# Kernel optimization log

Measured on AMD Instinct MI355X. Metric: run time of the kernel, lower is better.

The kernel has to match this reference:

```python
import jax, jax.numpy as jnp
import numpy as np

B, N, DIM = 4, 16384, 256
H, D, G = 8, 64, 32  # heads, dim_head, slice_num; inner = H*D = 512


def setup_inputs() -> dict:
    key = jax.random.key(0)
    ks = jax.random.split(key, 12)
    inner = H * D
    s = lambda fan_in: 1.0 / np.sqrt(fan_in)
    inp = {
        "x": jax.random.normal(ks[0], (B, N, DIM), jnp.float32),
        # weights stored (in, out) so forward is x @ W + b
        "Wfx": jax.random.uniform(ks[1], (DIM, inner), jnp.float32, -s(DIM), s(DIM)),
        "bfx": jnp.zeros((inner,), jnp.float32),
        "Wx": jax.random.uniform(ks[2], (DIM, inner), jnp.float32, -s(DIM), s(DIM)),
        "bx": jnp.zeros((inner,), jnp.float32),
        "Wslice": jnp.linalg.qr(jax.random.normal(ks[3], (D, G), jnp.float32))[0],  # orthogonal init
        "bslice": jnp.zeros((G,), jnp.float32),
        "temperature": jnp.full((1, H, 1, 1), 0.5, jnp.float32),
        "Wq": jax.random.uniform(ks[4], (D, D), jnp.float32, -s(D), s(D)),
        "Wk": jax.random.uniform(ks[5], (D, D), jnp.float32, -s(D), s(D)),
        "Wv": jax.random.uniform(ks[6], (D, D), jnp.float32, -s(D), s(D)),
        "Wout": jax.random.uniform(ks[7], (inner, DIM), jnp.float32, -s(inner), s(inner)),
        "bout": jnp.zeros((DIM,), jnp.float32),
    }
    return inp


def reference(x, Wfx, bfx, Wx, bx, Wslice, bslice, temperature, Wq, Wk, Wv, Wout, bout):
    b, n, _ = x.shape
    # projections -> [B, H, N, D]
    fx_mid = (x @ Wfx + bfx).reshape(b, n, H, D).transpose(0, 2, 1, 3)
    x_mid = (x @ Wx + bx).reshape(b, n, H, D).transpose(0, 2, 1, 3)
    # soft slice assignment: [B, H, N, G]
    slice_logits = (x_mid @ Wslice + bslice) / temperature
    slice_weights = jax.nn.softmax(slice_logits, axis=-1)
    slice_norm = slice_weights.sum(axis=2)  # [B, H, G]
    # soft pooling to G slice tokens: [B, H, G, D]
    slice_token = jnp.einsum("bhnd,bhng->bhgd", fx_mid, slice_weights)
    slice_token = slice_token / (slice_norm[..., None] + 1e-5)
    # tiny attention over G tokens
    q = slice_token @ Wq
    k = slice_token @ Wk
    v = slice_token @ Wv
    scores = jnp.einsum("bhgd,bhkd->bhgk", q, k) / jnp.sqrt(jnp.asarray(D, q.dtype))
    attn = jax.nn.softmax(scores, axis=-1)
    out_slice = jnp.einsum("bhgk,bhkd->bhgd", attn, v)
    # scatter back to N points: [B, H, N, D] -> [B, N, H*D]
    out_x = jnp.einsum("bhgd,bhng->bhnd", out_slice, slice_weights)
    out_x = out_x.transpose(0, 2, 1, 3).reshape(b, n, H * D)
    return out_x @ Wout + bout
```

## Files before the change

### kernel.cpp

```cpp
#include <hip/hip_runtime.h>


typedef unsigned short u16;
typedef __attribute__((ext_vector_type(8))) unsigned short ushort8v;
typedef __attribute__((ext_vector_type(4))) unsigned short ushort4v;
typedef __attribute__((ext_vector_type(8))) short short8v;
typedef __attribute__((ext_vector_type(4))) float f32x4;

constexpr int Nc = 16384;
constexpr int BNc = 65536;

__device__ inline float b2f(u16 v) {
    union { unsigned int u; float f; } t; t.u = ((unsigned int)v) << 16; return t.f;
}
__device__ inline u16 f2b(float f) {
    union { float f; unsigned int u; } t; t.f = f;
    unsigned int u = t.u;
    return (u16)((u + 0x7fffu + ((u >> 16) & 1u)) >> 16);
}

__global__ __launch_bounds__(256) void k0_fold(
    const float* __restrict__ Wx, const float* __restrict__ Wslice,
    const float* __restrict__ bx, const float* __restrict__ bslice,
    u16* __restrict__ WxsT, float* __restrict__ bxs)
{
    int blk = blockIdx.x, tid = threadIdx.x;
    int h = tid >> 5, g = tid & 31;
    if (blk < 256) {
        int k = blk;
        float acc = 0.f;
        for (int d = 0; d < 64; d++)
            acc += Wx[k * 512 + h * 64 + d] * Wslice[d * 32 + g];
        WxsT[tid * 256 + k] = f2b(acc);
    } else {
        float acc = 0.f;
        for (int d = 0; d < 64; d++)
            acc += bx[h * 64 + d] * Wslice[d * 32 + g];
        bxs[tid] = acc + bslice[g];
    }
}

__global__ __launch_bounds__(256) void kprep_wfx(const float* __restrict__ Wfx,
                                                 u16* __restrict__ WfxT)
{
    int n = blockIdx.x, k = threadIdx.x;
    WfxT[n * 256 + k] = f2b(Wfx[k * 512 + n]);
}

__global__ __launch_bounds__(256) void kfrag(const u16* __restrict__ Ball,
                                             u16* __restrict__ Bf)
{
    int g = blockIdx.x * 256 + threadIdx.x;
    int pair = g >> 6, lane = g & 63;
    int t = pair >> 3, c = pair & 7;
    int n = t * 16 + (lane & 15);
    int k = c * 32 + (lane >> 4) * 8;
    ushort8v v = *(const ushort8v*)(Ball + (size_t)n * 256 + k);
    *(ushort8v*)(Bf + (size_t)((c * 48 + t) * 64 + lane) * 8) = v;
}

__global__ __launch_bounds__(256, 4) void kproj(
    const float* __restrict__ x, const u16* __restrict__ Bf,
    const float* __restrict__ bfx, const float* __restrict__ bxs,
    const float* __restrict__ temp,
    u16* __restrict__ fxT, u16* __restrict__ swb, u16* __restrict__ swT)
{
    __shared__ u16 Bs[2][12288];
    int tid = threadIdx.x;
    int wave = tid >> 6, lane = tid & 63;
    int lm = lane & 15, quad = lane >> 4;
    int wr = wave & 1, wc = wave >> 1;
    int cg = blockIdx.y;
    int row0 = blockIdx.x * 32;
    int arow = row0 + wr * 16 + lm;

    const float* Aptr = x + (size_t)arow * 256 + quad * 8;
    const u16* BfW = Bf + (size_t)cg * 12288 + (size_t)(wave * 6) * 512 + lane * 8;

    f32x4 acc[12] = {};
    f32x4 a0 = *(const f32x4*)(Aptr);
    f32x4 a1 = *(const f32x4*)(Aptr + 4);

#pragma unroll
    for (int i = 0; i < 6; i++)
        __builtin_amdgcn_global_load_lds((const uint32_t*)(BfW + i * 512),
                                         (uint32_t*)(&Bs[0][(wave * 6 + i) * 512]),
                                         16, 0, 0);
    __syncthreads();

    int cur = 0;
    for (int c = 0; c < 8; c++) {
        if (c < 7) {
            const u16* src = BfW + (size_t)(c + 1) * 24576;
            u16* dst = &Bs[cur ^ 1][(wave * 6) * 512];
#pragma unroll
            for (int i = 0; i < 6; i++)
                __builtin_amdgcn_global_load_lds((const uint32_t*)(src + i * 512),
                                                 (uint32_t*)(dst + i * 512), 16, 0, 0);
        }
        ushort8v au;
#pragma unroll
        for (int j = 0; j < 4; j++) { au[j] = f2b(a0[j]); au[4 + j] = f2b(a1[j]); }
        short8v af = (short8v&)au;
        if (c < 7) {
            a0 = *(const f32x4*)(Aptr + c * 32 + 32);
            a1 = *(const f32x4*)(Aptr + c * 32 + 36);
        }
#pragma unroll
        for (int j = 0; j < 12; j++) {
            short8v bf = *(short8v*)&Bs[cur][(wc * 12 + j) * 512 + lane * 8];
            acc[j] = __builtin_amdgcn_mfma_f32_16x16x32_bf16(af, bf, acc[j], 0, 0, 0);
        }
        __syncthreads();
        cur ^= 1;
    }

    int nbase = row0 + wr * 16 + quad * 4;
    int tbase = cg * 24 + wc * 12;
    int nfx = (cg == 0) ? 12 : (wc == 0 ? 8 : 0);
#pragma unroll
    for (int j = 0; j < 12; j++) {
        if (j < nfx) {
            int cc = (tbase + j) * 16 + lm;
            float bv = bfx[cc];
            ushort4v o;
#pragma unroll
            for (int r = 0; r < 4; r++) o[r] = f2b(acc[j][r] + bv);
            *(ushort4v*)(fxT + (size_t)cc * 65536 + nbase) = o;
        }
    }

    if (cg == 1) {
        int b = row0 >> 14;
        int nlbase = (row0 & 16383) + wr * 16 + quad * 4;
        int nh = wc ? 6 : 2, h0 = wc ? 2 : 0, jb = wc ? 0 : 8;
#pragma unroll
        for (int hh = 0; hh < 6; hh++) {
            if (hh < nh) {
                int h = h0 + hh;
                float it = 1.0f / temp[h];
                float bv0 = bxs[h * 32 + lm];
                float bv1 = bxs[h * 32 + 16 + lm];
                f32x4 A0 = acc[jb + 2 * hh];
                f32x4 A1 = acc[jb + 2 * hh + 1];
                ushort4v p0, p1;
#pragma unroll
                for (int r = 0; r < 4; r++) {
                    float v0 = (A0[r] + bv0) * it;
                    float v1 = (A1[r] + bv1) * it;
                    float m = fmaxf(v0, v1);
                    m = fmaxf(m, __shfl_xor(m, 1));
                    m = fmaxf(m, __shfl_xor(m, 2));
                    m = fmaxf(m, __shfl_xor(m, 4));
                    m = fmaxf(m, __shfl_xor(m, 8));
                    float e0 = __expf(v0 - m), e1 = __expf(v1 - m);
                    float s = e0 + e1;
                    s += __shfl_xor(s, 1);
                    s += __shfl_xor(s, 2);
                    s += __shfl_xor(s, 4);
                    s += __shfl_xor(s, 8);
                    float rs = 1.0f / s;
                    float w0 = e0 * rs, w1 = e1 * rs;
                    int row = row0 + wr * 16 + quad * 4 + r;
                    swb[(size_t)row * 256 + h * 32 + lm] = f2b(w0);
                    swb[(size_t)row * 256 + h * 32 + 16 + lm] = f2b(w1);
                    p0[r] = f2b(w0); p1[r] = f2b(w1);
                }
                size_t gbase = (size_t)((b * 8 + h) * 32);
                *(ushort4v*)(swT + (gbase + lm) * 16384 + nlbase) = p0;
                *(ushort4v*)(swT + (gbase + 16 + lm) * 16384 + nlbase) = p1;
            }
        }
    }
}

__global__ __launch_bounds__(256, 4) void kout(
    const u16* __restrict__ swb, const u16* __restrict__ ZTf,
    const float* __restrict__ bout, float* __restrict__ out)
{
    __shared__ u16 Bs[16 * 512];
    int tid = threadIdx.x;
    int wave = tid >> 6, lane = tid & 63;
    int lm = lane & 15, quad = lane >> 4;
    int row0 = blockIdx.x * 64;

    const u16* Abase = swb + (size_t)(row0 + wave * 16 + lm) * 256 + quad * 8;
    const u16* Zb    = ZTf + (size_t)(row0 >> 14) * 65536;

    f32x4 acc[16] = {};
    short8v af = *(const short8v*)(Abase);
    for (int c = 0; c < 8; c++) {
        const u16* src = Zb + (size_t)c * 8192 + (size_t)(wave * 4) * 512 + lane * 8;
#pragma unroll
        for (int i = 0; i < 4; i++) {
            ushort8v v = *(const ushort8v*)(src + i * 512);
            *(ushort8v*)&Bs[(wave * 4 + i) * 512 + lane * 8] = v;
        }
        short8v a_cur = af;
        if (c < 7) af = *(const short8v*)(Abase + c * 32 + 32);
        __syncthreads();
#pragma unroll
        for (int j = 0; j < 16; j++) {
            short8v bf = *(short8v*)&Bs[j * 512 + lane * 8];
            acc[j] = __builtin_amdgcn_mfma_f32_16x16x32_bf16(a_cur, bf, acc[j], 0, 0, 0);
        }
        __syncthreads();
    }
#pragma unroll
    for (int j = 0; j < 16; j++) {
        int cc = j * 16 + lm;
        float bv = bout[cc];
#pragma unroll
        for (int r = 0; r < 4; r++)
            out[(size_t)(row0 + wave * 16 + quad * 4 + r) * 256 + cc] = acc[j][r] + bv;
    }
}

__global__ __launch_bounds__(256, 4) void k4_token_mfma(
    const u16* __restrict__ swT, const u16* __restrict__ fxT,
    float* __restrict__ token_part, float* __restrict__ norm_part)
{
    __shared__ u16 As[32 * 256];
    __shared__ u16 Bs_[64 * 256];
    int bh = blockIdx.x, ky = blockIdx.y;
    int b = bh >> 3, h = bh & 7;
    int tid = threadIdx.x, wave = tid >> 6, lane = tid & 63;
    int lm = lane & 15, quad = lane >> 4;
    int mt = wave & 1, dp = wave >> 1;
    int lh = lane >> 5, lb = lane & 31;

#pragma unroll
    for (int i = 0; i < 4; i++) {
        int s = wave * 4 + i;
        int r = 2 * s + lh;
        int sw = ((lb * 16) ^ ((r & 7) << 4)) >> 1;
        const u16* src = swT + (size_t)(bh * 32 + r) * 16384 + ky * 256 + sw;
        __builtin_amdgcn_global_load_lds((const uint32_t*)src,
                                         (uint32_t*)(&As[s * 512]), 16, 0, 0);
    }
#pragma unroll
    for (int i = 0; i < 8; i++) {
        int s = wave * 8 + i;
        int r = 2 * s + lh;
        int sw = ((lb * 16) ^ ((r & 7) << 4)) >> 1;
        const u16* src = fxT + (size_t)(h * 64 + r) * 65536 + (size_t)b * 16384
                         + ky * 256 + sw;
        __builtin_amdgcn_global_load_lds((const uint32_t*)src,
                                         (uint32_t*)(&Bs_[s * 512]), 16, 0, 0);
    }
    __syncthreads();

    int rA = mt * 16 + lm;
    int rB0 = dp * 32 + lm, rB1 = rB0 + 16;
    const char* Ab  = (const char*)As  + rA  * 512;
    const char* Bb0 = (const char*)Bs_ + rB0 * 512;
    const char* Bb1 = (const char*)Bs_ + rB1 * 512;
    int swA  = (rA  & 7) << 4;
    int swB0 = (rB0 & 7) << 4;
    int swB1 = (rB1 & 7) << 4;

    f32x4 acc0 = {}, acc1 = {};
    float nacc = 0.f;
#pragma unroll
    for (int kk = 0; kk < 8; kk++) {
        int base = kk * 64 + quad * 16;
        short8v af = *(const short8v*)(Ab  + (base ^ swA));
        short8v b0 = *(const short8v*)(Bb0 + (base ^ swB0));
        short8v b1 = *(const short8v*)(Bb1 + (base ^ swB1));
        acc0 = __builtin_amdgcn_mfma_f32_16x16x32_bf16(af, b0, acc0, 0, 0, 0);
        acc1 = __builtin_amdgcn_mfma_f32_16x16x32_bf16(af, b1, acc1, 0, 0, 0);
        if (dp == 0) {
            ushort8v au = (ushort8v&)af;
#pragma unroll
            for (int j = 0; j < 8; j++) nacc += b2f(au[j]);
        }
    }
    float* tp = token_part + ((size_t)(ky * 32 + bh)) * 2048;
#pragma unroll
    for (int r = 0; r < 4; r++) {
        int g = mt * 16 + quad * 4 + r;
        tp[g * 64 + dp * 32 + lm] = acc0[r];
        tp[g * 64 + dp * 32 + 16 + lm] = acc1[r];
    }
    if (dp == 0) {
        nacc += __shfl_xor(nacc, 16);
        nacc += __shfl_xor(nacc, 32);
        if (lane < 16)
            norm_part[(ky * 32 + bh) * 32 + mt * 16 + lm] = nacc;
    }
}

__global__ __launch_bounds__(256) void k4b_reduce(
    const float* __restrict__ tp, const float* __restrict__ np,
    float* __restrict__ tl)
{
    int t = blockIdx.x * 256 + threadIdx.x;
    int bh = t >> 11, e = t & 2047, g = e >> 6;
    float ts = 0.f, ns = 0.f;
    for (int ch = 0; ch < 64; ch++) {
        ts += tp[((size_t)(ch * 32 + bh)) * 2048 + e];
        ns += np[(ch * 32 + bh) * 32 + g];
    }
    tl[t] = ts / (ns + 1e-5f);
}

__global__ __launch_bounds__(256) void k5_attn(
    const float* __restrict__ tlg,
    const float* __restrict__ Wq, const float* __restrict__ Wk, const float* __restrict__ Wv,
    float* __restrict__ out_slice)
{
    __shared__ float tl[32][64];
    __shared__ float ql[32][64], kl[32][64], vl[32][64];
    __shared__ float sl[32][33];
    int bh = blockIdx.x, tid = threadIdx.x;
    const float* tk = tlg + (size_t)bh * 2048;

#pragma unroll
    for (int j = 0; j < 8; j++) {
        int idx = j * 256 + tid;
        tl[idx >> 6][idx & 63] = tk[idx];
    }
    __syncthreads();
#pragma unroll
    for (int j = 0; j < 8; j++) {
        int idx = j * 256 + tid;
        int g = idx >> 6, d = idx & 63;
        float aq = 0.f, ak = 0.f, av = 0.f;
        for (int e = 0; e < 64; e++) {
            float t = tl[g][e];
            aq += t * Wq[e * 64 + d];
            ak += t * Wk[e * 64 + d];
            av += t * Wv[e * 64 + d];
        }
        ql[g][d] = aq; kl[g][d] = ak; vl[g][d] = av;
    }
    __syncthreads();
#pragma unroll
    for (int j = 0; j < 4; j++) {
        int idx = j * 256 + tid;
        int gq = idx >> 5, gk = idx & 31;
        float s = 0.f;
        for (int d = 0; d < 64; d++) s += ql[gq][d] * kl[gk][d];
        sl[gq][gk] = s * 0.125f;
    }
    __syncthreads();
    if (tid < 32) {
        float m = -1e30f;
        for (int k2 = 0; k2 < 32; k2++) m = fmaxf(m, sl[tid][k2]);
        float s = 0.f;
        for (int k2 = 0; k2 < 32; k2++) { float e = __expf(sl[tid][k2] - m); sl[tid][k2] = e; s += e; }
        float r = 1.0f / s;
        for (int k2 = 0; k2 < 32; k2++) sl[tid][k2] *= r;
    }
    __syncthreads();
#pragma unroll
    for (int j = 0; j < 8; j++) {
        int idx = j * 256 + tid;
        int g = idx >> 6, d = idx & 63;
        float a = 0.f;
        for (int k2 = 0; k2 < 32; k2++) a += sl[g][k2] * vl[k2][d];
        out_slice[(size_t)bh * 2048 + idx] = a;
    }
}

__global__ __launch_bounds__(256) void kZ(
    const float* __restrict__ os, const float* __restrict__ Wout,
    u16* __restrict__ ZTf)
{
    int b = blockIdx.x, cb = blockIdx.y;
    int t = threadIdx.x;
    int c = cb * 16 + (t & 15), kq = t >> 4;
    int tile = c >> 4, lm = c & 15;
    for (int k = kq * 16; k < kq * 16 + 16; k++) {
        int h = k >> 5, g = k & 31;
        const float* osr = os + ((size_t)(b * 8 + h)) * 2048 + g * 64;
        float acc = 0.f;
        for (int d = 0; d < 64; d++)
            acc += osr[d] * Wout[(h * 64 + d) * 256 + c];
        int ch = k >> 5, quad = (k >> 3) & 3, jj = k & 7;
        int lane = quad * 16 + lm;
        ZTf[((size_t)((b * 8 + ch) * 16 + tile)) * 512 + lane * 8 + jj] = f2b(acc);
    }
}

extern "C" void kernel_launch(void* const* d_in, const int* in_sizes, int n_in,
                              void* d_out, int out_size, void* d_ws, size_t ws_size,
                              hipStream_t stream)
{
    const float* x      = (const float*)d_in[0];
    const float* Wfx    = (const float*)d_in[1];
    const float* bfx    = (const float*)d_in[2];
    const float* Wx     = (const float*)d_in[3];
    const float* bx     = (const float*)d_in[4];
    const float* Wslice = (const float*)d_in[5];
    const float* bslice = (const float*)d_in[6];
    const float* temp   = (const float*)d_in[7];
    const float* Wq     = (const float*)d_in[8];
    const float* Wk     = (const float*)d_in[9];
    const float* Wv     = (const float*)d_in[10];
    const float* Wout   = (const float*)d_in[11];
    const float* bout   = (const float*)d_in[12];

    char* ws = (char*)d_ws;
    size_t off = 0;
    auto alloc = [&](size_t bytes) {
        void* p = ws + off;
        off = (off + bytes + 255) & ~(size_t)255;
        return p;
    };
    u16*   fxT   = (u16*)  alloc((size_t)512 * BNc * 2);
    u16*   swb   = (u16*)  alloc((size_t)BNc * 256 * 2);
    u16*   swT   = (u16*)  alloc((size_t)1024 * Nc * 2);
    float* tp    = (float*)alloc((size_t)2048 * 2048 * 4);
    float* np    = (float*)alloc((size_t)2048 * 32 * 4);
    float* tl    = (float*)alloc(65536 * 4);
    float* osl   = (float*)alloc(65536 * 4);
    u16*   ZTf   = (u16*)  alloc(4 * 65536 * 2);
    u16*   Ball  = (u16*)  alloc((size_t)768 * 256 * 2);
    u16*   Bfrg  = (u16*)  alloc((size_t)768 * 256 * 2);
    float* bxs   = (float*)alloc(256 * 4);

    u16* WfxT = Ball;
    u16* WxsT = Ball + (size_t)512 * 256;

    k0_fold<<<257, 256, 0, stream>>>(Wx, Wslice, bx, bslice, WxsT, bxs);
    kprep_wfx<<<512, 256, 0, stream>>>(Wfx, WfxT);
    kfrag<<<96, 256, 0, stream>>>(Ball, Bfrg);

    kproj<<<dim3(2048, 2), 256, 0, stream>>>(x, Bfrg, bfx, bxs, temp, fxT, swb, swT);

    k4_token_mfma<<<dim3(32, 64), 256, 0, stream>>>(swT, fxT, tp, np);
    k4b_reduce<<<256, 256, 0, stream>>>(tp, np, tl);
    k5_attn<<<32, 256, 0, stream>>>(tl, Wq, Wk, Wv, osl);
    kZ<<<dim3(4, 16), 256, 0, stream>>>(osl, Wout, ZTf);

    kout<<<1024, 256, 0, stream>>>(swb, ZTf, bout, (float*)d_out);
}
```

Baseline: 376.0 us.

## Restructure projection GEMM to keep weights in registers and stage x in swizzled LDS

The projection kernel now uses 512-thread blocks over a 3-way column split. Each wave holds its two B column tiles in registers for the whole K loop, and the 32x256 x tile is converted to bf16 once and stored in XOR-swizzled shared memory. This replaces the double-buffered LDS streaming of weights and the per-wave fp32 A loads with their repeated bf16 conversion. Softmax output is now computed by a dedicated block group with one wave per head. In exchange, x is re-read by three block groups instead of two, and register pressure rises from the 16 held B fragments.

```diff
diff --git a/kernel.cpp b/kernel.cpp
--- a/kernel.cpp
+++ b/kernel.cpp
@@ -59,117 +59,110 @@
     *(ushort8v*)(Bf + (size_t)((c * 48 + t) * 64 + lane) * 8) = v;
 }
 
-__global__ __launch_bounds__(256, 4) void kproj(
+__global__ __launch_bounds__(512, 4) void kproj(
     const float* __restrict__ x, const u16* __restrict__ Bf,
     const float* __restrict__ bfx, const float* __restrict__ bxs,
     const float* __restrict__ temp,
     u16* __restrict__ fxT, u16* __restrict__ swb, u16* __restrict__ swT)
 {
-    __shared__ u16 Bs[2][12288];
+    __shared__ u16 As[32 * 256];
     int tid = threadIdx.x;
     int wave = tid >> 6, lane = tid & 63;
     int lm = lane & 15, quad = lane >> 4;
-    int wr = wave & 1, wc = wave >> 1;
-    int cg = blockIdx.y;
+    int tg = blockIdx.y;
     int row0 = blockIdx.x * 32;
-    int arow = row0 + wr * 16 + lm;
-
-    const float* Aptr = x + (size_t)arow * 256 + quad * 8;
-    const u16* BfW = Bf + (size_t)cg * 12288 + (size_t)(wave * 6) * 512 + lane * 8;
-
-    f32x4 acc[12] = {};
-    f32x4 a0 = *(const f32x4*)(Aptr);
-    f32x4 a1 = *(const f32x4*)(Aptr + 4);
-
-#pragma unroll
-    for (int i = 0; i < 6; i++)
-        __builtin_amdgcn_global_load_lds((const uint32_t*)(BfW + i * 512),
-                                         (uint32_t*)(&Bs[0][(wave * 6 + i) * 512]),
-                                         16, 0, 0);
-    __syncthreads();
-
-    int cur = 0;
+    int T0 = tg * 16 + 2 * wave;
+
+    short8v breg0[8], breg1[8];
+#pragma unroll
     for (int c = 0; c < 8; c++) {
-        if (c < 7) {
-            const u16* src = BfW + (size_t)(c + 1) * 24576;
-            u16* dst = &Bs[cur ^ 1][(wave * 6) * 512];
-#pragma unroll
-            for (int i = 0; i < 6; i++)
-                __builtin_amdgcn_global_load_lds((const uint32_t*)(src + i * 512),
-                                                 (uint32_t*)(dst + i * 512), 16, 0, 0);
-        }
-        ushort8v au;
-#pragma unroll
-        for (int j = 0; j < 4; j++) { au[j] = f2b(a0[j]); au[4 + j] = f2b(a1[j]); }
-        short8v af = (short8v&)au;
-        if (c < 7) {
-            a0 = *(const f32x4*)(Aptr + c * 32 + 32);
-            a1 = *(const f32x4*)(Aptr + c * 32 + 36);
-        }
-#pragma unroll
-        for (int j = 0; j < 12; j++) {
-            short8v bf = *(short8v*)&Bs[cur][(wc * 12 + j) * 512 + lane * 8];
-            acc[j] = __builtin_amdgcn_mfma_f32_16x16x32_bf16(af, bf, acc[j], 0, 0, 0);
-        }
-        __syncthreads();
-        cur ^= 1;
-    }
-
-    int nbase = row0 + wr * 16 + quad * 4;
-    int tbase = cg * 24 + wc * 12;
-    int nfx = (cg == 0) ? 12 : (wc == 0 ? 8 : 0);
-#pragma unroll
-    for (int j = 0; j < 12; j++) {
-        if (j < nfx) {
-            int cc = (tbase + j) * 16 + lm;
+        breg0[c] = *(const short8v*)(Bf + (size_t)((c * 48 + T0) * 64 + lane) * 8);
+        breg1[c] = *(const short8v*)(Bf + (size_t)((c * 48 + T0 + 1) * 64 + lane) * 8);
+    }
+
+    {
+        int row = tid >> 4, colg = tid & 15;
+        const f32x4* src = (const f32x4*)(x + (size_t)(row0 + row) * 256 + colg * 16);
+        f32x4 v0 = src[0], v1 = src[1], v2 = src[2], v3 = src[3];
+        ushort8v o0, o1;
+#pragma unroll
+        for (int j = 0; j < 4; j++) {
+            o0[j] = f2b(v0[j]); o0[4 + j] = f2b(v1[j]);
+            o1[j] = f2b(v2[j]); o1[4 + j] = f2b(v3[j]);
+        }
+        int sw = (row & 7) << 4;
+        char* base = (char*)As + row * 512;
+        *(ushort8v*)(base + ((colg * 32) ^ sw)) = o0;
+        *(ushort8v*)(base + ((colg * 32 + 16) ^ sw)) = o1;
+    }
+    __syncthreads();
+
+    f32x4 acc00 = {}, acc01 = {}, acc10 = {}, acc11 = {};
+    int swl = (lm & 7) << 4;
+    const char* Arow0 = (const char*)As + lm * 512;
+    const char* Arow1 = (const char*)As + (16 + lm) * 512;
+#pragma unroll
+    for (int c = 0; c < 8; c++) {
+        int off = (c * 64 + quad * 16) ^ swl;
+        short8v af0 = *(const short8v*)(Arow0 + off);
+        short8v af1 = *(const short8v*)(Arow1 + off);
+        acc00 = __builtin_amdgcn_mfma_f32_16x16x32_bf16(af0, breg0[c], acc00, 0, 0, 0);
+        acc10 = __builtin_amdgcn_mfma_f32_16x16x32_bf16(af1, breg0[c], acc10, 0, 0, 0);
+        acc01 = __builtin_amdgcn_mfma_f32_16x16x32_bf16(af0, breg1[c], acc01, 0, 0, 0);
+        acc11 = __builtin_amdgcn_mfma_f32_16x16x32_bf16(af1, breg1[c], acc11, 0, 0, 0);
+    }
+
+    if (tg < 2) {
+        int nbase = row0 + quad * 4;
+#pragma unroll
+        for (int i = 0; i < 2; i++) {
+            int cc = (T0 + i) * 16 + lm;
             float bv = bfx[cc];
-            ushort4v o;
-#pragma unroll
-            for (int r = 0; r < 4; r++) o[r] = f2b(acc[j][r] + bv);
-            *(ushort4v*)(fxT + (size_t)cc * 65536 + nbase) = o;
-        }
-    }
-
-    if (cg == 1) {
+            const f32x4& a0 = i ? acc01 : acc00;
+            const f32x4& a1 = i ? acc11 : acc10;
+            ushort4v o0, o1;
+#pragma unroll
+            for (int r = 0; r < 4; r++) { o0[r] = f2b(a0[r] + bv); o1[r] = f2b(a1[r] + bv); }
+            *(ushort4v*)(fxT + (size_t)cc * 65536 + nbase) = o0;
+            *(ushort4v*)(fxT + (size_t)cc * 65536 + nbase + 16) = o1;
+        }
+    } else {
+        int h = wave;
         int b = row0 >> 14;
-        int nlbase = (row0 & 16383) + wr * 16 + quad * 4;
-        int nh = wc ? 6 : 2, h0 = wc ? 2 : 0, jb = wc ? 0 : 8;
-#pragma unroll
-        for (int hh = 0; hh < 6; hh++) {
-            if (hh < nh) {
-                int h = h0 + hh;
-                float it = 1.0f / temp[h];
-                float bv0 = bxs[h * 32 + lm];
-                float bv1 = bxs[h * 32 + 16 + lm];
-                f32x4 A0 = acc[jb + 2 * hh];
-                f32x4 A1 = acc[jb + 2 * hh + 1];
-                ushort4v p0, p1;
-#pragma unroll
-                for (int r = 0; r < 4; r++) {
-                    float v0 = (A0[r] + bv0) * it;
-                    float v1 = (A1[r] + bv1) * it;
-                    float m = fmaxf(v0, v1);
-                    m = fmaxf(m, __shfl_xor(m, 1));
-                    m = fmaxf(m, __shfl_xor(m, 2));
-                    m = fmaxf(m, __shfl_xor(m, 4));
-                    m = fmaxf(m, __shfl_xor(m, 8));
-                    float e0 = __expf(v0 - m), e1 = __expf(v1 - m);
-                    float s = e0 + e1;
-                    s += __shfl_xor(s, 1);
-                    s += __shfl_xor(s, 2);
-                    s += __shfl_xor(s, 4);
-                    s += __shfl_xor(s, 8);
-                    float rs = 1.0f / s;
-                    float w0 = e0 * rs, w1 = e1 * rs;
-                    int row = row0 + wr * 16 + quad * 4 + r;
-                    swb[(size_t)row * 256 + h * 32 + lm] = f2b(w0);
-                    swb[(size_t)row * 256 + h * 32 + 16 + lm] = f2b(w1);
-                    p0[r] = f2b(w0); p1[r] = f2b(w1);
-                }
-                size_t gbase = (size_t)((b * 8 + h) * 32);
-                *(ushort4v*)(swT + (gbase + lm) * 16384 + nlbase) = p0;
-                *(ushort4v*)(swT + (gbase + 16 + lm) * 16384 + nlbase) = p1;
+        float it = 1.0f / temp[h];
+        float bv0 = bxs[h * 32 + lm];
+        float bv1 = bxs[h * 32 + 16 + lm];
+        size_t gbase = (size_t)((b * 8 + h) * 32);
+#pragma unroll
+        for (int rf = 0; rf < 2; rf++) {
+            const f32x4& A0 = rf ? acc10 : acc00;
+            const f32x4& A1 = rf ? acc11 : acc01;
+            int nlbase = (row0 & 16383) + rf * 16 + quad * 4;
+            ushort4v p0, p1;
+#pragma unroll
+            for (int r = 0; r < 4; r++) {
+                float v0 = (A0[r] + bv0) * it;
+                float v1 = (A1[r] + bv1) * it;
+                float m = fmaxf(v0, v1);
+                m = fmaxf(m, __shfl_xor(m, 1));
+                m = fmaxf(m, __shfl_xor(m, 2));
+                m = fmaxf(m, __shfl_xor(m, 4));
+                m = fmaxf(m, __shfl_xor(m, 8));
+                float e0 = __expf(v0 - m), e1 = __expf(v1 - m);
+                float s = e0 + e1;
+                s += __shfl_xor(s, 1);
+                s += __shfl_xor(s, 2);
+                s += __shfl_xor(s, 4);
+                s += __shfl_xor(s, 8);
+                float rs = 1.0f / s;
+                float w0 = e0 * rs, w1 = e1 * rs;
+                int row = row0 + rf * 16 + quad * 4 + r;
+                swb[(size_t)row * 256 + h * 32 + lm] = f2b(w0);
+                swb[(size_t)row * 256 + h * 32 + 16 + lm] = f2b(w1);
+                p0[r] = f2b(w0); p1[r] = f2b(w1);
             }
+            *(ushort4v*)(swT + (gbase + lm) * 16384 + nlbase) = p0;
+            *(ushort4v*)(swT + (gbase + 16 + lm) * 16384 + nlbase) = p1;
         }
     }
 }
@@ -427,7 +420,7 @@
     kprep_wfx<<<512, 256, 0, stream>>>(Wfx, WfxT);
     kfrag<<<96, 256, 0, stream>>>(Ball, Bfrg);
 
-    kproj<<<dim3(2048, 2), 256, 0, stream>>>(x, Bfrg, bfx, bxs, temp, fxT, swb, swT);
+    kproj<<<dim3(2048, 3), 512, 0, stream>>>(x, Bfrg, bfx, bxs, temp, fxT, swb, swT);
 
     k4_token_mfma<<<dim3(32, 64), 256, 0, stream>>>(swT, fxT, tp, np);
     k4b_reduce<<<256, 256, 0, stream>>>(tp, np, tl);
```

After: 338.5 us. -10.0%, faster.
